# Optimization experiments

Hardware: AMD Instinct MI355X
Metric: run time of the kernel (lower is better)

Reference implementation:

```python
import jax, jax.numpy as jnp
import numpy as np

N_NODES = 100000
N_EDGES = 1600000
D_IN = 128
D_OUT = 128


def setup_inputs() -> dict:
    key = jax.random.key(0)
    ks = jax.random.split(key, 7)
    x = jax.random.normal(ks[0], (N_NODES, D_IN), dtype=jnp.float32)
    y = jax.random.normal(ks[1], (N_NODES, D_OUT), dtype=jnp.float32)
    edge_src = jax.random.randint(ks[2], (N_EDGES,), 0, N_NODES, dtype=jnp.int32)
    edge_dst = jax.random.randint(ks[3], (N_EDGES,), 0, N_NODES, dtype=jnp.int32)
    adj_vals = jax.random.uniform(ks[4], (N_EDGES,), dtype=jnp.float32)
    weight = jax.random.normal(ks[5], (D_IN, D_OUT), dtype=jnp.float32) * (1.0 / np.sqrt(D_IN))
    bias = jax.random.normal(ks[6], (D_OUT,), dtype=jnp.float32) * 0.01
    return {"x": x, "y": y, "edge_src": edge_src, "edge_dst": edge_dst,
            "adj_vals": adj_vals, "weight": weight, "bias": bias}


def reference(x, y, edge_src, edge_dst, adj_vals, weight, bias):
    # GraphConvolution: support = x @ W ; out = spmm(adj, support) + bias
    support = x @ weight                      # [N, d_out]
    msgs = support[edge_src] * adj_vals[:, None]   # [E, d_out] gather + scale
    agg = jax.ops.segment_sum(msgs, edge_dst, num_segments=N_NODES)  # [N, d_out]
    gc_out = agg + bias
    # ResGCN epilogue: relu(gc_out + y); dropout is identity in eval (p=0.0)
    return jax.nn.relu(gc_out + y)
```

## Files before the change

kernel.cpp:

```cpp
#include <hip/hip_runtime.h>

#define D 128
#define CE 8192
#define NB_MAX 1024
#define MAXC 512
#define EBUF 3072
#define CHUNK 1024
#define WTP 136


typedef __attribute__((ext_vector_type(8))) short bf16x8;
typedef __attribute__((ext_vector_type(4))) float f32x4;

__device__ __forceinline__ unsigned short f2bf(float f) {
  unsigned u = __float_as_uint(f);
  unsigned r = (u + 0x7fffu + ((u >> 16) & 1u)) >> 16;
  return (unsigned short)r;
}

__device__ __forceinline__ int wave_iscan(int v) {
  const int lane = threadIdx.x & 63;
#pragma unroll
  for (int off = 1; off < 64; off <<= 1) {
    int u = __shfl_up(v, off, 64);
    if (lane >= off) v += u;
  }
  return v;
}

__device__ __forceinline__ int seg_find(const int* pref, int nC, int i) {
  int lo = 0, hi = nC;
  while (hi - lo > 1) {
    int mid = (lo + hi) >> 1;
    if (pref[mid] <= i) lo = mid; else hi = mid;
  }
  return lo;
}

__global__ __launch_bounds__(1024) void sort_convert_kernel(
    const int* __restrict__ src, const int* __restrict__ dst,
    const float* __restrict__ adj, int2* __restrict__ edges,
    unsigned short* __restrict__ ofs, int nE, int nB, int nC,
    const float4* __restrict__ x4, ushort4* __restrict__ xb4, int n4,
    int nxblk, const float* __restrict__ w, unsigned short* __restrict__ wt) {
  __shared__ int2 stage[CE];
  __shared__ int h[NB_MAX + 4];
  __shared__ int wsum[16];
  const int bid = blockIdx.x;
  const int t = threadIdx.x;

  if (bid >= nC) {
    int b2 = bid - nC;
    if (b2 < nxblk) {
      int i = b2 * 1024 + t;
      if (i < n4) {
        float4 v = x4[i];
        ushort4 r;
        r.x = f2bf(v.x);
        r.y = f2bf(v.y);
        r.z = f2bf(v.z);
        r.w = f2bf(v.w);
        xb4[i] = r;
      }
    } else {
      int idx = (b2 - nxblk) * 1024 + t;
      if (idx < D * D) {
        int n = idx >> 7, k = idx & 127;
        wt[n * WTP + k] = f2bf(w[k * D + n]);
      }
    }
    return;
  }

  const int c = bid;
  const int e0 = c * CE;
  const int n = min(CE, nE - e0);
  const int lane = t & 63, wid = t >> 6;

  for (int i = t; i < NB_MAX + 4; i += 1024) h[i] = 0;
  __syncthreads();

  int dreg[8];
#pragma unroll
  for (int k = 0; k < 8; ++k) {
    int i = k * 1024 + t;
    if (i < n) {
      int d = dst[e0 + i];
      int rank = atomicAdd(&h[d >> 7], 1);
      dreg[k] = d | (rank << 17);
    }
  }
  __syncthreads();

  int v = h[t];
  int inc = wave_iscan(v);
  if (lane == 63) wsum[wid] = inc;
  __syncthreads();
  if (wid == 0) {
    int p = (lane < 16) ? wsum[lane] : 0;
    int pi = wave_iscan(p);
    if (lane < 16) wsum[lane] = pi;
  }
  __syncthreads();
  h[t] = inc - v + (wid ? wsum[wid - 1] : 0);
  __syncthreads();

  unsigned short* o = ofs + (size_t)c * (nB + 1);
  for (int i = t; i <= nB; i += 1024)
    o[i] = (unsigned short)(i < NB_MAX ? h[i] : n);

#pragma unroll
  for (int k = 0; k < 8; ++k) {
    int i = k * 1024 + t;
    if (i < n) {
      int dr = dreg[k];
      int d = dr & 0x1FFFF;
      int rank = ((unsigned)dr) >> 17;
      int pos = h[d >> 7] + rank;
      int2 ev;
      ev.x = src[e0 + i] | ((d & 127) << 17);
      ev.y = __float_as_int(adj[e0 + i]);
      stage[pos] = ev;
    }
  }
  __syncthreads();

  for (int i = t; i < n; i += 1024) edges[e0 + i] = stage[i];
}

__global__ __launch_bounds__(256) void bucket_gather_kernel(
    const int2* __restrict__ tmp, const unsigned short* __restrict__ ofs,
    const uint2* __restrict__ xb, char* out, int nC, int nB, int nNodes) {
  __shared__ int2 ebuf[EBUF];
  __shared__ int segst[MAXC];
  __shared__ int pref[MAXC + 1];
  __shared__ int cnt[128];
  __shared__ int cur[128];
  __shared__ int sstart[128];
  __shared__ int w4[4];
  const int t = threadIdx.x;
  const int b = blockIdx.x;
  const int lane = t & 63, wid = t >> 6;

  const int c0 = 2 * t, c1 = 2 * t + 1;
  int n0 = 0, n1 = 0;
  if (c0 < nC) {
    int s0 = ofs[(size_t)c0 * (nB + 1) + b];
    int s1 = ofs[(size_t)c0 * (nB + 1) + b + 1];
    segst[c0] = c0 * CE + s0;
    n0 = s1 - s0;
  }
  if (c1 < nC) {
    int s0 = ofs[(size_t)c1 * (nB + 1) + b];
    int s1 = ofs[(size_t)c1 * (nB + 1) + b + 1];
    segst[c1] = c1 * CE + s0;
    n1 = s1 - s0;
  }
  int tt = n0 + n1;
  int inc = wave_iscan(tt);
  if (lane == 63) w4[wid] = inc;
  __syncthreads();
  int add = 0;
  for (int i = 0; i < wid; ++i) add += w4[i];
  int incl = inc + add;
  int excl = incl - tt;
  if (c0 < nC) pref[c0] = excl;
  if (c1 < nC) pref[c1] = excl + n0;
  if (t == 255) pref[nC] = incl;
  __syncthreads();
  const int m = pref[nC];

  const int gi = t >> 5;
  const int q = t & 31;
  float4 acc[16];
#pragma unroll
  for (int k = 0; k < 16; ++k) acc[k] = make_float4(0.f, 0.f, 0.f, 0.f);

  for (int w0 = 0; w0 < m; w0 += EBUF) {
    const int w1 = min(m, w0 + EBUF);
    if (t < 128) cnt[t] = 0;
    __syncthreads();

    for (int i = w0 + t; i < w1; i += 256) {
      int lo = seg_find(pref, nC, i);
      int sx = ((const int*)tmp)[(size_t)(segst[lo] + (i - pref[lo])) * 2];
      atomicAdd(&cnt[(sx >> 17) & 127], 1);
    }
    __syncthreads();

    int cv = (t < 128) ? cnt[t] : 0;
    int cinc = wave_iscan(cv);
    if (t == 63) w4[0] = cinc;
    __syncthreads();
    int cst = cinc - cv + ((t >= 64 && t < 128) ? w4[0] : 0);
    if (t < 128) {
      sstart[t] = cst;
      cur[t] = cst;
    }
    __syncthreads();

    for (int i = w0 + t; i < w1; i += 256) {
      int lo = seg_find(pref, nC, i);
      int2 ev = tmp[segst[lo] + (i - pref[lo])];
      int pos = atomicAdd(&cur[(ev.x >> 17) & 127], 1);
      ebuf[pos] = ev;
    }
    __syncthreads();

#pragma unroll
    for (int k = 0; k < 16; ++k) {
      const int dl = gi * 16 + k;
      int j = sstart[dl];
      const int e = cur[dl];
      for (; j + 3 < e; j += 4) {
        int2 e0 = ebuf[j], e1 = ebuf[j + 1], e2 = ebuf[j + 2], e3 = ebuf[j + 3];
        float a0 = __int_as_float(e0.y), a1 = __int_as_float(e1.y);
        float a2 = __int_as_float(e2.y), a3 = __int_as_float(e3.y);
        uint2 v0 = xb[(size_t)(e0.x & 0x1FFFF) * 32 + q];
        uint2 v1 = xb[(size_t)(e1.x & 0x1FFFF) * 32 + q];
        uint2 v2 = xb[(size_t)(e2.x & 0x1FFFF) * 32 + q];
        uint2 v3 = xb[(size_t)(e3.x & 0x1FFFF) * 32 + q];
        acc[k].x = fmaf(a0, __uint_as_float(v0.x << 16), acc[k].x);
        acc[k].y = fmaf(a0, __uint_as_float(v0.x & 0xffff0000u), acc[k].y);
        acc[k].z = fmaf(a0, __uint_as_float(v0.y << 16), acc[k].z);
        acc[k].w = fmaf(a0, __uint_as_float(v0.y & 0xffff0000u), acc[k].w);
        acc[k].x = fmaf(a1, __uint_as_float(v1.x << 16), acc[k].x);
        acc[k].y = fmaf(a1, __uint_as_float(v1.x & 0xffff0000u), acc[k].y);
        acc[k].z = fmaf(a1, __uint_as_float(v1.y << 16), acc[k].z);
        acc[k].w = fmaf(a1, __uint_as_float(v1.y & 0xffff0000u), acc[k].w);
        acc[k].x = fmaf(a2, __uint_as_float(v2.x << 16), acc[k].x);
        acc[k].y = fmaf(a2, __uint_as_float(v2.x & 0xffff0000u), acc[k].y);
        acc[k].z = fmaf(a2, __uint_as_float(v2.y << 16), acc[k].z);
        acc[k].w = fmaf(a2, __uint_as_float(v2.y & 0xffff0000u), acc[k].w);
        acc[k].x = fmaf(a3, __uint_as_float(v3.x << 16), acc[k].x);
        acc[k].y = fmaf(a3, __uint_as_float(v3.x & 0xffff0000u), acc[k].y);
        acc[k].z = fmaf(a3, __uint_as_float(v3.y << 16), acc[k].z);
        acc[k].w = fmaf(a3, __uint_as_float(v3.y & 0xffff0000u), acc[k].w);
      }
      for (; j < e; ++j) {
        int2 e0 = ebuf[j];
        float a0 = __int_as_float(e0.y);
        uint2 v0 = xb[(size_t)(e0.x & 0x1FFFF) * 32 + q];
        acc[k].x = fmaf(a0, __uint_as_float(v0.x << 16), acc[k].x);
        acc[k].y = fmaf(a0, __uint_as_float(v0.x & 0xffff0000u), acc[k].y);
        acc[k].z = fmaf(a0, __uint_as_float(v0.y << 16), acc[k].z);
        acc[k].w = fmaf(a0, __uint_as_float(v0.y & 0xffff0000u), acc[k].w);
      }
    }
    __syncthreads();
  }

#pragma unroll
  for (int k = 0; k < 16; ++k) {
    int g = b * 128 + gi * 16 + k;
    if (g < nNodes) {
      uint2 pk;
      pk.x = (unsigned)f2bf(acc[k].x) | ((unsigned)f2bf(acc[k].y) << 16);
      pk.y = (unsigned)f2bf(acc[k].z) | ((unsigned)f2bf(acc[k].w) << 16);
      ((uint2*)(out + (size_t)g * 512))[q] = pk;
    }
  }
}

__global__ __launch_bounds__(256) void gemm_mfma_kernel(
    const char* aggb, const unsigned short* __restrict__ wt,
    const float* __restrict__ y, const float* __restrict__ bias,
    float* out, int nNodes) {
  __shared__ unsigned short sWt[D * WTP];
  const int t = threadIdx.x;
  for (int i = t; i < D * WTP / 8; i += 256)
    ((int4*)sWt)[i] = ((const int4*)wt)[i];
  __syncthreads();

  const int w = t >> 6, l = t & 63;
  const int quad = l >> 4, m = l & 15;
  const int row0 = blockIdx.x * 128 + w * 32;

  const int ar0 = min(row0 + m, nNodes - 1);
  const int ar1 = min(row0 + 16 + m, nNodes - 1);
  const char* pa0 = aggb + (size_t)ar0 * 512;
  const char* pa1 = aggb + (size_t)ar1 * 512;

  f32x4 acc0[8], acc1[8];
#pragma unroll
  for (int nt = 0; nt < 8; ++nt) {
    acc0[nt] = (f32x4){0.f, 0.f, 0.f, 0.f};
    acc1[nt] = (f32x4){0.f, 0.f, 0.f, 0.f};
  }

#pragma unroll
  for (int ks = 0; ks < 4; ++ks) {
    const int kof = ks * 32 + quad * 8;
    bf16x8 a0 = *(const bf16x8*)(pa0 + kof * 2);
    bf16x8 a1 = *(const bf16x8*)(pa1 + kof * 2);
#pragma unroll
    for (int nt = 0; nt < 8; ++nt) {
      bf16x8 b = *(const bf16x8*)&sWt[(nt * 16 + m) * WTP + kof];
      acc0[nt] = __builtin_amdgcn_mfma_f32_16x16x32_bf16(a0, b, acc0[nt], 0, 0, 0);
      acc1[nt] = __builtin_amdgcn_mfma_f32_16x16x32_bf16(a1, b, acc1[nt], 0, 0, 0);
    }
  }

  float bv[8];
#pragma unroll
  for (int nt = 0; nt < 8; ++nt) bv[nt] = bias[nt * 16 + m];

#pragma unroll
  for (int s = 0; s < 2; ++s) {
#pragma unroll
    for (int r = 0; r < 4; ++r) {
      int row = row0 + s * 16 + quad * 4 + r;
      if (row >= nNodes) continue;
      const float* yr = y + (size_t)row * D;
      float* orow = out + (size_t)row * D;
#pragma unroll
      for (int nt = 0; nt < 8; ++nt) {
        int c = nt * 16 + m;
        float v = (s == 0 ? acc0[nt][r] : acc1[nt][r]) + yr[c] + bv[nt];
        orow[c] = fmaxf(v, 0.f);
      }
    }
  }
}

__global__ __launch_bounds__(256) void zero_counts_kernel(int* __restrict__ c, int n) {
  int i = blockIdx.x * 256 + threadIdx.x;
  if (i < n) c[i] = 0;
}

__global__ __launch_bounds__(256) void hist_kernel(
    const int* __restrict__ dst, int* __restrict__ counts, int nE) {
  int e = blockIdx.x * 256 + threadIdx.x;
  if (e < nE) atomicAdd(&counts[dst[e]], 1);
}

__global__ __launch_bounds__(256) void scan_partial_kernel(
    const int* __restrict__ counts, int* __restrict__ chunk_sum, int n) {
  __shared__ int sdata[256];
  int b = blockIdx.x, t = threadIdx.x;
  int base = b * CHUNK + t * 4;
  int s = 0;
#pragma unroll
  for (int k = 0; k < 4; ++k) {
    int i = base + k;
    if (i < n) s += counts[i];
  }
  sdata[t] = s;
  __syncthreads();
  for (int off = 128; off > 0; off >>= 1) {
    if (t < off) sdata[t] += sdata[t + off];
    __syncthreads();
  }
  if (t == 0) chunk_sum[b] = sdata[0];
}

__global__ void scan_chunks_kernel(const int* __restrict__ chunk_sum,
                                   int* __restrict__ chunk_off,
                                   int* __restrict__ row_start, int nchunks, int n) {
  if (threadIdx.x == 0 && blockIdx.x == 0) {
    int run = 0;
    for (int i = 0; i < nchunks; ++i) {
      chunk_off[i] = run;
      run += chunk_sum[i];
    }
    row_start[n] = run;
  }
}

__global__ __launch_bounds__(256) void scan_final_kernel(
    const int* __restrict__ counts, const int* __restrict__ chunk_off,
    int* __restrict__ row_start, int* __restrict__ cursor, int n) {
  __shared__ int sdata[256];
  int b = blockIdx.x, t = threadIdx.x;
  int base = b * CHUNK + t * 4;
  int c[4] = {0, 0, 0, 0};
#pragma unroll
  for (int k = 0; k < 4; ++k) {
    int i = base + k;
    if (i < n) c[k] = counts[i];
  }
  int tsum = c[0] + c[1] + c[2] + c[3];
  sdata[t] = tsum;
  __syncthreads();
  for (int off = 1; off < 256; off <<= 1) {
    int v = (t >= off) ? sdata[t - off] : 0;
    __syncthreads();
    sdata[t] += v;
    __syncthreads();
  }
  int run = sdata[t] - tsum + chunk_off[b];
#pragma unroll
  for (int k = 0; k < 4; ++k) {
    int i = base + k;
    if (i < n) {
      row_start[i] = run;
      cursor[i] = run;
      run += c[k];
    }
  }
}

__global__ __launch_bounds__(256) void scatter_sort_kernel(
    const int* __restrict__ src, const int* __restrict__ dst,
    const float* __restrict__ adj, int* __restrict__ cursor,
    int2* __restrict__ edges, int nE) {
  int e = blockIdx.x * 256 + threadIdx.x;
  if (e >= nE) return;
  int d = dst[e];
  int2 ev;
  ev.x = src[e];
  ev.y = __float_as_int(adj[e]);
  int pos = atomicAdd(&cursor[d], 1);
  edges[pos] = ev;
}

__global__ __launch_bounds__(256) void gather_fp32_kernel(
    const float* __restrict__ x, const int* __restrict__ row_start,
    const int2* __restrict__ edges, float* __restrict__ out, int nNodes) {
  int g = (blockIdx.x * 256 + threadIdx.x) >> 5;
  int q = threadIdx.x & 31;
  if (g >= nNodes) return;
  int beg = row_start[g], end = row_start[g + 1];
  const float4* x4 = (const float4*)x;
  float4 acc = make_float4(0.f, 0.f, 0.f, 0.f);
  for (int j = beg; j < end; ++j) {
    int2 e0 = edges[j];
    float a0 = __int_as_float(e0.y);
    float4 v0 = x4[(size_t)e0.x * 32 + q];
    acc.x = fmaf(a0, v0.x, acc.x);
    acc.y = fmaf(a0, v0.y, acc.y);
    acc.z = fmaf(a0, v0.z, acc.z);
    acc.w = fmaf(a0, v0.w, acc.w);
  }
  ((float4*)out)[(size_t)g * 32 + q] = acc;
}

__global__ __launch_bounds__(256) void zero_kernel(float4* __restrict__ out, int n4) {
  int i = blockIdx.x * 256 + threadIdx.x;
  if (i < n4) out[i] = make_float4(0.f, 0.f, 0.f, 0.f);
}

__global__ __launch_bounds__(256) void scatter_atomic_kernel(
    const float* __restrict__ x, const int* __restrict__ src,
    const int* __restrict__ dst, const float* __restrict__ adj,
    float* __restrict__ out, int nE) {
  int tid = blockIdx.x * 256 + threadIdx.x;
  int e = tid >> 5;
  int q = tid & 31;
  if (e >= nE) return;
  int s = src[e];
  int d = dst[e];
  float a = adj[e];
  float4 v = ((const float4*)x)[(size_t)s * 32 + q];
  float* o = out + (size_t)d * D + q * 4;
  atomicAdd(o + 0, v.x * a);
  atomicAdd(o + 1, v.y * a);
  atomicAdd(o + 2, v.z * a);
  atomicAdd(o + 3, v.w * a);
}

__global__ __launch_bounds__(256) void gemm_fused_kernel(
    float* __restrict__ out, const float* __restrict__ w,
    const float* __restrict__ y, const float* __restrict__ bias, int nrows) {
  __shared__ float sW[D * D];
  __shared__ float sA[32 * D];
  const int tid = threadIdx.x;
  const int row0 = blockIdx.x * 32;

  const float4* w4 = (const float4*)w;
  float4* sW4 = (float4*)sW;
  for (int i = tid; i < D * D / 4; i += 256) sW4[i] = w4[i];

  const int nrow_blk = min(32, nrows - row0);
  const float4* out4_base = (const float4*)(out + (size_t)row0 * D);
  float4* sA4 = (float4*)sA;
  for (int i = tid; i < nrow_blk * 32; i += 256) sA4[i] = out4_base[i];
  __syncthreads();

  const int cg = tid & 31;
  const int rs = tid >> 5;

  float4 acc[4];
#pragma unroll
  for (int r = 0; r < 4; ++r) acc[r] = make_float4(0.f, 0.f, 0.f, 0.f);

#pragma unroll 4
  for (int k4 = 0; k4 < 32; ++k4) {
    float4 wv0 = sW4[(k4 * 4 + 0) * 32 + cg];
    float4 wv1 = sW4[(k4 * 4 + 1) * 32 + cg];
    float4 wv2 = sW4[(k4 * 4 + 2) * 32 + cg];
    float4 wv3 = sW4[(k4 * 4 + 3) * 32 + cg];
#pragma unroll
    for (int r = 0; r < 4; ++r) {
      float4 xv = sA4[(rs + r * 8) * 32 + k4];
      acc[r].x = fmaf(xv.x, wv0.x, acc[r].x);
      acc[r].y = fmaf(xv.x, wv0.y, acc[r].y);
      acc[r].z = fmaf(xv.x, wv0.z, acc[r].z);
      acc[r].w = fmaf(xv.x, wv0.w, acc[r].w);
      acc[r].x = fmaf(xv.y, wv1.x, acc[r].x);
      acc[r].y = fmaf(xv.y, wv1.y, acc[r].y);
      acc[r].z = fmaf(xv.y, wv1.z, acc[r].z);
      acc[r].w = fmaf(xv.y, wv1.w, acc[r].w);
      acc[r].x = fmaf(xv.z, wv2.x, acc[r].x);
      acc[r].y = fmaf(xv.z, wv2.y, acc[r].y);
      acc[r].z = fmaf(xv.z, wv2.z, acc[r].z);
      acc[r].w = fmaf(xv.z, wv2.w, acc[r].w);
      acc[r].x = fmaf(xv.w, wv3.x, acc[r].x);
      acc[r].y = fmaf(xv.w, wv3.y, acc[r].y);
      acc[r].z = fmaf(xv.w, wv3.z, acc[r].z);
      acc[r].w = fmaf(xv.w, wv3.w, acc[r].w);
    }
  }

  const float4* y4 = (const float4*)y;
  const float4* b4 = (const float4*)bias;
  float4* o4 = (float4*)out;
  float4 bv = b4[cg];
#pragma unroll
  for (int r = 0; r < 4; ++r) {
    int row = row0 + rs + r * 8;
    if (row < nrows) {
      float4 yv = y4[(size_t)row * 32 + cg];
      float4 res;
      res.x = fmaxf(acc[r].x + yv.x + bv.x, 0.f);
      res.y = fmaxf(acc[r].y + yv.y + bv.y, 0.f);
      res.z = fmaxf(acc[r].z + yv.z + bv.z, 0.f);
      res.w = fmaxf(acc[r].w + yv.w + bv.w, 0.f);
      o4[(size_t)row * 32 + cg] = res;
    }
  }
}

extern "C" void kernel_launch(void* const* d_in, const int* in_sizes, int n_in,
                              void* d_out, int out_size, void* d_ws, size_t ws_size,
                              hipStream_t stream) {
  const float* x    = (const float*)d_in[0];
  const float* y    = (const float*)d_in[1];
  const int*   esrc = (const int*)d_in[2];
  const int*   edst = (const int*)d_in[3];
  const float* adj  = (const float*)d_in[4];
  const float* w    = (const float*)d_in[5];
  const float* bias = (const float*)d_in[6];
  float* out = (float*)d_out;

  const int nNodes = in_sizes[0] / D;
  const int nE = in_sizes[2];
  const int n4 = nNodes * (D / 4);
  const int nB = (nNodes + 127) >> 7;
  const int nC = (nE + CE - 1) / CE;

  const size_t ofs_bytes = (((size_t)nC * (nB + 1) * 2) + 15) & ~(size_t)15;
  const size_t wt_bytes  = (size_t)D * WTP * 2;
  const size_t tmp_bytes = (size_t)nC * CE * 8;
  const size_t xb_bytes  = (size_t)nNodes * D * 2;
  const size_t need1 = ofs_bytes + wt_bytes + tmp_bytes + xb_bytes;

  const int nchunks = (nNodes + CHUNK - 1) / CHUNK;
  const size_t e2_bytes  = (size_t)nE * 8;
  const size_t int_bytes = (size_t)(3 * nNodes + 1 + 2 * nchunks) * 4;
  const size_t need2 = e2_bytes + int_bytes;

  if (ws_size >= need1 && nNodes <= NB_MAX * 128 && nC <= MAXC) {
    char* p = (char*)d_ws;
    unsigned short* ofs = (unsigned short*)p;   p += ofs_bytes;
    unsigned short* wt = (unsigned short*)p;    p += wt_bytes;
    int2* tmp = (int2*)p;                       p += tmp_bytes;
    ushort4* xb4 = (ushort4*)p;

    const int nxblk = (n4 + 1023) / 1024;
    const int wtblk = (D * D + 1023) / 1024;
    sort_convert_kernel<<<nC + nxblk + wtblk, 1024, 0, stream>>>(
        esrc, edst, adj, tmp, ofs, nE, nB, nC,
        (const float4*)x, xb4, n4, nxblk, w, wt);
    bucket_gather_kernel<<<nB, 256, 0, stream>>>(
        tmp, ofs, (const uint2*)xb4, (char*)d_out, nC, nB, nNodes);
    gemm_mfma_kernel<<<(nNodes + 127) / 128, 256, 0, stream>>>(
        (const char*)d_out, wt, y, bias, out, nNodes);
  } else if (ws_size >= need2) {
    char* base = (char*)d_ws;
    int2* edges = (int2*)base;
    int* counts = (int*)(base + e2_bytes);
    int* row_start = counts + nNodes;
    int* cursor = row_start + nNodes + 1;
    int* chunk_sum = cursor + nNodes;
    int* chunk_off = chunk_sum + nchunks;

    zero_counts_kernel<<<(nNodes + 255) / 256, 256, 0, stream>>>(counts, nNodes);
    hist_kernel<<<(nE + 255) / 256, 256, 0, stream>>>(edst, counts, nE);
    scan_partial_kernel<<<nchunks, 256, 0, stream>>>(counts, chunk_sum, nNodes);
    scan_chunks_kernel<<<1, 64, 0, stream>>>(chunk_sum, chunk_off, row_start,
                                             nchunks, nNodes);
    scan_final_kernel<<<nchunks, 256, 0, stream>>>(counts, chunk_off, row_start,
                                                   cursor, nNodes);
    scatter_sort_kernel<<<(nE + 255) / 256, 256, 0, stream>>>(
        esrc, edst, adj, cursor, edges, nE);
    gather_fp32_kernel<<<(nNodes * 32 + 255) / 256, 256, 0, stream>>>(
        x, row_start, edges, out, nNodes);
    gemm_fused_kernel<<<(nNodes + 31) / 32, 256, 0, stream>>>(out, w, y, bias,
                                                              nNodes);
  } else {
    zero_kernel<<<(n4 + 255) / 256, 256, 0, stream>>>((float4*)out, n4);
    scatter_atomic_kernel<<<((size_t)nE * 32 + 255) / 256, 256, 0, stream>>>(
        x, esrc, edst, adj, out, nE);
    gemm_fused_kernel<<<(nNodes + 31) / 32, 256, 0, stream>>>(out, w, y, bias,
                                                              nNodes);
  }
}
```

Baseline: 296.1 us.

## Reorder to GEMM-first then gather with fused bias, residual and ReLU epilogue

Swaps the order of operations: x@W is computed first into a bf16 support buffer written in place over the converted x, then the edge gather aggregates support rows and applies bias, residual y and ReLU directly. This removes the bf16 aggregate round trip through the output buffer and the separate GEMM epilogue pass over y and out. The trade-off is an extra bf16 rounding of support before aggregation, which changes numerics slightly, and an in-place overwrite that relies on each block reading its rows before writing them.

```diff
diff --git a/kernel.cpp b/kernel.cpp
--- a/kernel.cpp
+++ b/kernel.cpp
@@ -128,9 +128,77 @@
   for (int i = t; i < n; i += 1024) edges[e0 + i] = stage[i];
 }
 
-__global__ __launch_bounds__(256) void bucket_gather_kernel(
+__global__ __launch_bounds__(256) void gemm_support_kernel(
+    unsigned short* __restrict__ xb, const unsigned short* __restrict__ wt,
+    int nNodes) {
+  __shared__ unsigned short sWt[D * WTP];
+  const int t = threadIdx.x;
+  for (int i = t; i < D * WTP / 8; i += 256)
+    ((int4*)sWt)[i] = ((const int4*)wt)[i];
+  __syncthreads();
+
+  const int w = t >> 6, l = t & 63;
+  const int quad = l >> 4, m = l & 15;
+  const int row0 = blockIdx.x * 128 + w * 32;
+  const int ar0 = min(row0 + m, nNodes - 1);
+  const int ar1 = min(row0 + 16 + m, nNodes - 1);
+  const unsigned short* pa0 = xb + (size_t)ar0 * D;
+  const unsigned short* pa1 = xb + (size_t)ar1 * D;
+
+  bf16x8 a0[4], a1[4];
+#pragma unroll
+  for (int ks = 0; ks < 4; ++ks) {
+    const int kof = ks * 32 + quad * 8;
+    a0[ks] = *(const bf16x8*)(pa0 + kof);
+    a1[ks] = *(const bf16x8*)(pa1 + kof);
+  }
+
+  f32x4 acc0[8], acc1[8];
+#pragma unroll
+  for (int nt = 0; nt < 8; ++nt) {
+    acc0[nt] = (f32x4){0.f, 0.f, 0.f, 0.f};
+    acc1[nt] = (f32x4){0.f, 0.f, 0.f, 0.f};
+  }
+
+#pragma unroll
+  for (int ks = 0; ks < 4; ++ks) {
+    const int kof = ks * 32 + quad * 8;
+#pragma unroll
+    for (int nt = 0; nt < 8; ++nt) {
+      bf16x8 b = *(const bf16x8*)&sWt[(nt * 16 + m) * WTP + kof];
+      acc0[nt] = __builtin_amdgcn_mfma_f32_16x16x32_bf16(a0[ks], b, acc0[nt], 0, 0, 0);
+      acc1[nt] = __builtin_amdgcn_mfma_f32_16x16x32_bf16(a1[ks], b, acc1[nt], 0, 0, 0);
+    }
+  }
+  __syncthreads();
+
+#pragma unroll
+  for (int s = 0; s < 2; ++s) {
+#pragma unroll
+    for (int r = 0; r < 4; ++r) {
+      int rl = w * 32 + s * 16 + quad * 4 + r;
+#pragma unroll
+      for (int nt = 0; nt < 8; ++nt)
+        sWt[rl * WTP + nt * 16 + m] =
+            f2bf(s == 0 ? acc0[nt][r] : acc1[nt][r]);
+    }
+  }
+  __syncthreads();
+
+  const int base = blockIdx.x * 128;
+  for (int c = t; c < 128 * 16; c += 256) {
+    int rl = c >> 4, co = c & 15;
+    int g = base + rl;
+    if (g < nNodes)
+      *(int4*)&xb[(size_t)g * D + co * 8] = *(const int4*)&sWt[rl * WTP + co * 8];
+  }
+}
+
+__global__ __launch_bounds__(256) void gather_final_kernel(
     const int2* __restrict__ tmp, const unsigned short* __restrict__ ofs,
-    const uint2* __restrict__ xb, char* out, int nC, int nB, int nNodes) {
+    const uint2* __restrict__ sb, const float* __restrict__ y,
+    const float* __restrict__ bias, float* __restrict__ out,
+    int nC, int nB, int nNodes) {
   __shared__ int2 ebuf[EBUF];
   __shared__ int segst[MAXC];
   __shared__ int pref[MAXC + 1];
@@ -216,10 +284,10 @@
         int2 e0 = ebuf[j], e1 = ebuf[j + 1], e2 = ebuf[j + 2], e3 = ebuf[j + 3];
         float a0 = __int_as_float(e0.y), a1 = __int_as_float(e1.y);
         float a2 = __int_as_float(e2.y), a3 = __int_as_float(e3.y);
-        uint2 v0 = xb[(size_t)(e0.x & 0x1FFFF) * 32 + q];
-        uint2 v1 = xb[(size_t)(e1.x & 0x1FFFF) * 32 + q];
-        uint2 v2 = xb[(size_t)(e2.x & 0x1FFFF) * 32 + q];
-        uint2 v3 = xb[(size_t)(e3.x & 0x1FFFF) * 32 + q];
+        uint2 v0 = sb[(size_t)(e0.x & 0x1FFFF) * 32 + q];
+        uint2 v1 = sb[(size_t)(e1.x & 0x1FFFF) * 32 + q];
+        uint2 v2 = sb[(size_t)(e2.x & 0x1FFFF) * 32 + q];
+        uint2 v3 = sb[(size_t)(e3.x & 0x1FFFF) * 32 + q];
         acc[k].x = fmaf(a0, __uint_as_float(v0.x << 16), acc[k].x);
         acc[k].y = fmaf(a0, __uint_as_float(v0.x & 0xffff0000u), acc[k].y);
         acc[k].z = fmaf(a0, __uint_as_float(v0.y << 16), acc[k].z);
@@ -240,7 +308,7 @@
       for (; j < e; ++j) {
         int2 e0 = ebuf[j];
         float a0 = __int_as_float(e0.y);
-        uint2 v0 = xb[(size_t)(e0.x & 0x1FFFF) * 32 + q];
+        uint2 v0 = sb[(size_t)(e0.x & 0x1FFFF) * 32 + q];
         acc[k].x = fmaf(a0, __uint_as_float(v0.x << 16), acc[k].x);
         acc[k].y = fmaf(a0, __uint_as_float(v0.x & 0xffff0000u), acc[k].y);
         acc[k].z = fmaf(a0, __uint_as_float(v0.y << 16), acc[k].z);
@@ -250,75 +318,18 @@
     __syncthreads();
   }
 
+  const float4 bv = *(const float4*)&bias[q * 4];
 #pragma unroll
   for (int k = 0; k < 16; ++k) {
     int g = b * 128 + gi * 16 + k;
     if (g < nNodes) {
-      uint2 pk;
-      pk.x = (unsigned)f2bf(acc[k].x) | ((unsigned)f2bf(acc[k].y) << 16);
-      pk.y = (unsigned)f2bf(acc[k].z) | ((unsigned)f2bf(acc[k].w) << 16);
-      ((uint2*)(out + (size_t)g * 512))[q] = pk;
-    }
-  }
-}
-
-__global__ __launch_bounds__(256) void gemm_mfma_kernel(
-    const char* aggb, const unsigned short* __restrict__ wt,
-    const float* __restrict__ y, const float* __restrict__ bias,
-    float* out, int nNodes) {
-  __shared__ unsigned short sWt[D * WTP];
-  const int t = threadIdx.x;
-  for (int i = t; i < D * WTP / 8; i += 256)
-    ((int4*)sWt)[i] = ((const int4*)wt)[i];
-  __syncthreads();
-
-  const int w = t >> 6, l = t & 63;
-  const int quad = l >> 4, m = l & 15;
-  const int row0 = blockIdx.x * 128 + w * 32;
-
-  const int ar0 = min(row0 + m, nNodes - 1);
-  const int ar1 = min(row0 + 16 + m, nNodes - 1);
-  const char* pa0 = aggb + (size_t)ar0 * 512;
-  const char* pa1 = aggb + (size_t)ar1 * 512;
-
-  f32x4 acc0[8], acc1[8];
-#pragma unroll
-  for (int nt = 0; nt < 8; ++nt) {
-    acc0[nt] = (f32x4){0.f, 0.f, 0.f, 0.f};
-    acc1[nt] = (f32x4){0.f, 0.f, 0.f, 0.f};
-  }
-
-#pragma unroll
-  for (int ks = 0; ks < 4; ++ks) {
-    const int kof = ks * 32 + quad * 8;
-    bf16x8 a0 = *(const bf16x8*)(pa0 + kof * 2);
-    bf16x8 a1 = *(const bf16x8*)(pa1 + kof * 2);
-#pragma unroll
-    for (int nt = 0; nt < 8; ++nt) {
-      bf16x8 b = *(const bf16x8*)&sWt[(nt * 16 + m) * WTP + kof];
-      acc0[nt] = __builtin_amdgcn_mfma_f32_16x16x32_bf16(a0, b, acc0[nt], 0, 0, 0);
-      acc1[nt] = __builtin_amdgcn_mfma_f32_16x16x32_bf16(a1, b, acc1[nt], 0, 0, 0);
-    }
-  }
-
-  float bv[8];
-#pragma unroll
-  for (int nt = 0; nt < 8; ++nt) bv[nt] = bias[nt * 16 + m];
-
-#pragma unroll
-  for (int s = 0; s < 2; ++s) {
-#pragma unroll
-    for (int r = 0; r < 4; ++r) {
-      int row = row0 + s * 16 + quad * 4 + r;
-      if (row >= nNodes) continue;
-      const float* yr = y + (size_t)row * D;
-      float* orow = out + (size_t)row * D;
-#pragma unroll
-      for (int nt = 0; nt < 8; ++nt) {
-        int c = nt * 16 + m;
-        float v = (s == 0 ? acc0[nt][r] : acc1[nt][r]) + yr[c] + bv[nt];
-        orow[c] = fmaxf(v, 0.f);
-      }
+      float4 yv = *(const float4*)&y[(size_t)g * D + q * 4];
+      float4 res;
+      res.x = fmaxf(acc[k].x + yv.x + bv.x, 0.f);
+      res.y = fmaxf(acc[k].y + yv.y + bv.y, 0.f);
+      res.z = fmaxf(acc[k].z + yv.z + bv.z, 0.f);
+      res.w = fmaxf(acc[k].w + yv.w + bv.w, 0.f);
+      *(float4*)&out[(size_t)g * D + q * 4] = res;
     }
   }
 }
@@ -565,17 +576,17 @@
     unsigned short* ofs = (unsigned short*)p;   p += ofs_bytes;
     unsigned short* wt = (unsigned short*)p;    p += wt_bytes;
     int2* tmp = (int2*)p;                       p += tmp_bytes;
-    ushort4* xb4 = (ushort4*)p;
+    unsigned short* xb = (unsigned short*)p;
 
     const int nxblk = (n4 + 1023) / 1024;
     const int wtblk = (D * D + 1023) / 1024;
     sort_convert_kernel<<<nC + nxblk + wtblk, 1024, 0, stream>>>(
         esrc, edst, adj, tmp, ofs, nE, nB, nC,
-        (const float4*)x, xb4, n4, nxblk, w, wt);
-    bucket_gather_kernel<<<nB, 256, 0, stream>>>(
-        tmp, ofs, (const uint2*)xb4, (char*)d_out, nC, nB, nNodes);
-    gemm_mfma_kernel<<<(nNodes + 127) / 128, 256, 0, stream>>>(
-        (const char*)d_out, wt, y, bias, out, nNodes);
+        (const float4*)x, (ushort4*)xb, n4, nxblk, w, wt);
+    gemm_support_kernel<<<(nNodes + 127) / 128, 256, 0, stream>>>(
+        xb, wt, nNodes);
+    gather_final_kernel<<<nB, 256, 0, stream>>>(
+        tmp, ofs, (const uint2*)xb, y, bias, out, nC, nB, nNodes);
   } else if (ws_size >= need2) {
     char* base = (char*)d_ws;
     int2* edges = (int2*)base;
```

New measurement: 257.8 us. 12.9% less time.
